# Kernel optimization log

Hardware: AMD Instinct MI355X
Metric: run time of the kernel (lower is better)

The kernel has to match this reference:

```python
import jax, jax.numpy as jnp
import numpy as np

N = 1_500_000
NUM_VOXELS = 262_144  # static segment count (replaces torch.unique's dynamic voxel count)
VSIZE = np.array([0.32, 0.32, 0.32], np.float32)
PC_MIN = np.array([-74.88, -74.88, -2.0], np.float32)
GRID = np.array([468, 468, 32], np.int64)
BN_EPS = 1e-3


def setup_inputs() -> dict:
    rng = np.random.default_rng(0)
    # points uniformly inside the point-cloud range -> the range mask is all-true
    xyz = rng.uniform(PC_MIN, PC_MIN + VSIZE * GRID - 1e-3, size=(N, 3)).astype(np.float32)
    feats = rng.uniform(0.0, 1.0, size=(N, 1)).astype(np.float32)
    coords = np.floor((xyz - PC_MIN) / VSIZE).astype(np.int64)
    merge = coords[:, 0] * (GRID[1] * GRID[2]) + coords[:, 1] * GRID[2] + coords[:, 2]
    unq_inv = (merge % NUM_VOXELS).astype(np.int32)  # static-size stand-in for unique inverse ids
    key = jax.random.key(0)
    k1, k2 = jax.random.split(key)
    return {
        'points_xyz': jnp.asarray(xyz),
        'point_feats': jnp.asarray(feats),
        'w1': jax.random.normal(k1, (11, 32), jnp.float32) * 0.1,
        'g1': jnp.ones((32,), jnp.float32),
        'b1': jnp.zeros((32,), jnp.float32),
        'w2': jax.random.normal(k2, (64, 64), jnp.float32) * 0.1,
        'g2': jnp.ones((64,), jnp.float32),
        'b2': jnp.zeros((64,), jnp.float32),
        'unq_inv': jnp.asarray(unq_inv),
    }


def _pfn(x, w, g, b, unq_inv):
    # Linear(bias=False) -> BatchNorm1d(train-mode batch stats, eps=1e-3) -> ReLU -> scatter_max
    y = x @ w
    mu = jnp.mean(y, axis=0)
    var = jnp.var(y, axis=0)
    y = (y - mu) * jax.lax.rsqrt(var + BN_EPS) * g + b
    y = jax.nn.relu(y)
    # relu output >= 0; clamp empty segments (-inf) to 0, matching torch_scatter's zero fill
    y_max = jnp.maximum(jax.ops.segment_max(y, unq_inv, num_segments=NUM_VOXELS), 0.0)
    return y, y_max


def reference(points_xyz, point_feats, w1, g1, b1, w2, g2, b2, unq_inv):
    vsize = jnp.asarray(VSIZE)
    pc_min = jnp.asarray(PC_MIN)
    coords = jnp.floor((points_xyz - pc_min) / vsize)  # [N,3] float voxel coords

    # scatter_mean of xyz per voxel -> cluster-relative offsets
    ones = jnp.ones((points_xyz.shape[0],), points_xyz.dtype)
    cnt = jax.ops.segment_sum(ones, unq_inv, num_segments=NUM_VOXELS)
    vsum = jax.ops.segment_sum(points_xyz, unq_inv, num_segments=NUM_VOXELS)
    vmean = vsum / jnp.maximum(cnt, 1.0)[:, None]
    f_cluster = points_xyz - vmean[unq_inv]

    # offset from voxel center
    f_center = points_xyz - (coords * vsize + vsize * 0.5 + pc_min)
    dist = jnp.linalg.norm(points_xyz, axis=1, keepdims=True)

    feat = jnp.concatenate([points_xyz, point_feats, f_cluster, f_center, dist], axis=-1)  # [N,11]

    x, x_max = _pfn(feat, w1, g1, b1, unq_inv)            # [N,32], [V,32]
    x = jnp.concatenate([x, x_max[unq_inv]], axis=1)       # [N,64]
    _, out = _pfn(x, w2, g2, b2, unq_inv)                  # [V,64] pillar features
    return out
```

## Files before the change

### kernel.cpp

```cpp
#include <hip/hip_runtime.h>

#define NPTS 1500000
#define NVOX 262144
#define BN_EPS 1e-3f
#define PAD 1500160
#define NB_PT 5860
#define NB_L2 11720

typedef __attribute__((ext_vector_type(8))) short bf16x8;
typedef __attribute__((ext_vector_type(4))) float f32x4;

__device__ __forceinline__ unsigned fkey(float f) {
    unsigned u = __float_as_uint(f);
    return u ^ ((unsigned)(((int)u) >> 31) | 0x80000000u);
}
__device__ __forceinline__ float funkey(unsigned k) {
    unsigned u = (k & 0x80000000u) ? (k ^ 0x80000000u) : ~k;
    return __uint_as_float(u);
}
#define KEY_NEG_INF 0x007FFFFFu

__device__ __forceinline__ float bf2f(unsigned short h) {
    union { unsigned u; float f; } x; x.u = ((unsigned)h) << 16; return x.f;
}
__device__ __forceinline__ unsigned short f2bf(float f) {
    union { float f; unsigned u; } x; x.f = f;
    unsigned r = x.u + 0x7FFFu + ((x.u >> 16) & 1u);
    return (unsigned short)(r >> 16);
}

__device__ __forceinline__ void make_feat(float x, float y, float z, float w,
                                          float mx, float my, float mz, float* f) {
    const float VS = 0.32f;
    const float PMX = -74.88f, PMY = -74.88f, PMZ = -2.0f;
    f[0] = x; f[1] = y; f[2] = z; f[3] = w;
    f[4] = x - mx; f[5] = y - my; f[6] = z - mz;
    float cx = floorf((x - PMX) / VS);
    float cy = floorf((y - PMY) / VS);
    float cz = floorf((z - PMZ) / VS);
    f[7] = x - (cx * VS + 0.5f * VS + PMX);
    f[8] = y - (cy * VS + 0.5f * VS + PMY);
    f[9] = z - (cz * VS + 0.5f * VS + PMZ);
    f[10] = sqrtf(x * x + y * y + z * z);
}

__global__ void k_init(unsigned* __restrict__ okeys, unsigned* __restrict__ xmraw,
                       int* __restrict__ cntv, float* __restrict__ zf,
                       int* __restrict__ svid, const float* __restrict__ w2,
                       uint4* __restrict__ wfrag) {
    long t0 = (long)blockIdx.x * 256 + threadIdx.x;
    long st = (long)gridDim.x * 256;
    uint4 kneg = make_uint4(KEY_NEG_INF, KEY_NEG_INF, KEY_NEG_INF, KEY_NEG_INF);
    for (long i = t0; i < (long)NVOX * 16; i += st) ((uint4*)okeys)[i] = kneg;
    for (long i = t0; i < (long)NVOX * 8; i += st) ((uint4*)xmraw)[i] = kneg;
    for (long i = t0; i < NVOX / 4; i += st) ((int4*)cntv)[i] = make_int4(0, 0, 0, 0);
    for (long i = t0; i < (1024 + 256 * 64 + 256 * 128) / 4; i += st)
        ((float4*)zf)[i] = make_float4(0.f, 0.f, 0.f, 0.f);
    if (t0 < PAD - NPTS) svid[NPTS + t0] = -1;
    if (blockIdx.x == 0 && threadIdx.x < 64) {
        int l = threadIdx.x;
        int lr = l & 15, lk = l >> 4;
        #pragma unroll
        for (int nt = 0; nt < 4; ++nt)
            #pragma unroll
            for (int kt = 0; kt < 2; ++kt) {
                int col = nt * 16 + lr;
                int kb = kt * 32 + lk * 8;
                unsigned u[4];
                #pragma unroll
                for (int j = 0; j < 4; ++j) {
                    float a = w2[(kb + 2 * j) * 64 + col];
                    float b = w2[(kb + 2 * j + 1) * 64 + col];
                    u[j] = (unsigned)f2bf(a) | ((unsigned)f2bf(b) << 16);
                }
                wfrag[(nt * 2 + kt) * 64 + l] = make_uint4(u[0], u[1], u[2], u[3]);
            }
    }
}

__global__ void k_hist(const int* __restrict__ unq, int* __restrict__ cntv) {
    int i = blockIdx.x * blockDim.x + threadIdx.x;
    if (i < NPTS) atomicAdd(&cntv[unq[i]], 1);
}

__global__ void k_scanA(const int* __restrict__ cntv, int* __restrict__ startv,
                        int* __restrict__ bsum) {
    __shared__ int lds[256];
    int t = threadIdx.x;
    int idx4 = blockIdx.x * 256 + t;
    int4 cv = ((const int4*)cntv)[idx4];
    int s0 = cv.x, s1 = s0 + cv.y, s2 = s1 + cv.z, T = s2 + cv.w;
    lds[t] = T;
    __syncthreads();
    for (int o = 1; o < 256; o <<= 1) {
        int v = (t >= o) ? lds[t - o] : 0;
        __syncthreads();
        lds[t] += v;
        __syncthreads();
    }
    int excl = lds[t] - T;
    int4 ov; ov.x = excl; ov.y = excl + s0; ov.z = excl + s1; ov.w = excl + s2;
    ((int4*)startv)[idx4] = ov;
    if (t == 255) bsum[blockIdx.x] = lds[255];
}

__global__ void k_scanB(int* __restrict__ bsum) {
    __shared__ int lds[256];
    int t = threadIdx.x;
    int b = bsum[t];
    lds[t] = b;
    __syncthreads();
    for (int o = 1; o < 256; o <<= 1) {
        int v = (t >= o) ? lds[t - o] : 0;
        __syncthreads();
        lds[t] += v;
        __syncthreads();
    }
    bsum[t] = lds[t] - b;
}

__global__ void k_scanC(int* __restrict__ startv, int* __restrict__ offv,
                        const int* __restrict__ bsum) {
    int t = threadIdx.x;
    int idx4 = blockIdx.x * 256 + t;
    int add = bsum[blockIdx.x];
    int4 v = ((int4*)startv)[idx4];
    v.x += add; v.y += add; v.z += add; v.w += add;
    ((int4*)startv)[idx4] = v;
    ((int4*)offv)[idx4] = v;
}

__global__ void k_scatter2(const float* __restrict__ xyz, const float* __restrict__ pf,
                           const int* __restrict__ unq, int* __restrict__ offv,
                           float4* __restrict__ spts, int* __restrict__ svid) {
    int i = blockIdx.x * blockDim.x + threadIdx.x;
    if (i >= NPTS) return;
    int v = unq[i];
    int pos = atomicAdd(&offv[v], 1);
    float4 p;
    p.x = xyz[3 * i + 0]; p.y = xyz[3 * i + 1]; p.z = xyz[3 * i + 2]; p.w = pf[i];
    spts[pos] = p;
    svid[pos] = v;
}

__global__ void k_vmean2(const float4* __restrict__ spts, const int* __restrict__ cntv,
                         const int* __restrict__ startv, float4* __restrict__ vmeanv) {
    int v = blockIdx.x * 256 + threadIdx.x;
    int cnt = cntv[v];
    if (!cnt) return;
    int st = startv[v];
    float sx = 0, sy = 0, sz = 0;
    for (int j = 0; j < cnt; ++j) {
        float4 p = spts[st + j];
        sx += p.x; sy += p.y; sz += p.z;
    }
    float inv = 1.0f / (float)cnt;
    vmeanv[v] = make_float4(sx * inv, sy * inv, sz * inv, 0.f);
}

__device__ __forceinline__ void flush32(int v, float m, bool atom, int c,
                                        unsigned* __restrict__ xm) {
    if ((unsigned)v >= (unsigned)NVOX) return;
    if (atom) atomicMax(&xm[(size_t)v * 32 + c], fkey(m));
    else xm[(size_t)v * 32 + c] = fkey(m);
}
__device__ __forceinline__ void flush64(int v, float m, bool atom, int c,
                                        unsigned* __restrict__ ok) {
    if ((unsigned)v >= (unsigned)NVOX) return;
    if (atom) atomicMax(&ok[(size_t)v * 64 + c], fkey(m));
    else ok[(size_t)v * 64 + c] = fkey(m);
}

__global__ __launch_bounds__(256) void k_passA(
    const float4* __restrict__ spts, const int* __restrict__ svid,
    const float4* __restrict__ vmeanv, const float* __restrict__ w1,
    unsigned* __restrict__ xmraw, float* __restrict__ spart1) {
    __shared__ float ylds[256 * 32];
    __shared__ int vlds[256];
    __shared__ float accs[64];
    __shared__ int hv[8][32]; __shared__ float hk[8][32];
    __shared__ int tv[8][32]; __shared__ float tk[8][32];
    __shared__ unsigned char sgl[8][32];
    int t = threadIdx.x;
    if (t < 64) accs[t] = 0.f;
    long grow = (long)blockIdx.x * 256 + t;
    int vid = (grow < NPTS) ? svid[grow] : -1;
    vlds[t] = vid;
    float yv[32];
    #pragma unroll
    for (int c = 0; c < 32; ++c) yv[c] = 0.f;
    if (vid >= 0) {
        float4 p = spts[grow];
        float4 vm = vmeanv[vid];
        float f[11];
        make_feat(p.x, p.y, p.z, p.w, vm.x, vm.y, vm.z, f);
        #pragma unroll
        for (int k = 0; k < 11; ++k) {
            float fk = f[k];
            #pragma unroll
            for (int c = 0; c < 32; ++c) yv[c] = fmaf(fk, w1[k * 32 + c], yv[c]);
        }
    }
    f32x4* yr = (f32x4*)&ylds[t * 32];
    #pragma unroll
    for (int q = 0; q < 8; ++q) {
        f32x4 vv = {yv[4 * q], yv[4 * q + 1], yv[4 * q + 2], yv[4 * q + 3]};
        yr[q ^ (t & 7)] = vv;
    }
    __syncthreads();
    {
        int c = t & 31, ck = t >> 5;
        int cq = c >> 2, ce = c & 3;
        float sa = 0.f, sq = 0.f;
        int cur_v = -2; float cur_m = 0.f;
        int hvv = -2; float hkk = 0.f; bool fd = false;
        for (int s = 0; s < 32; ++s) {
            int r = ck * 32 + s;
            float y = ylds[r * 32 + 4 * (cq ^ (r & 7)) + ce];
            int v = vlds[r];
            sa += y; sq += y * y;
            if (s == 0) { cur_v = v; cur_m = y; }
            else if (v == cur_v) cur_m = fmaxf(cur_m, y);
            else {
                if (!fd) { hvv = cur_v; hkk = cur_m; fd = true; }
                else if ((unsigned)cur_v < (unsigned)NVOX)
                    xmraw[(size_t)cur_v * 32 + c] = fkey(cur_m);
                cur_v = v; cur_m = y;
            }
        }
        hv[ck][c] = fd ? hvv : cur_v; hk[ck][c] = fd ? hkk : cur_m;
        tv[ck][c] = cur_v; tk[ck][c] = cur_m; sgl[ck][c] = fd ? 0 : 1;
        atomicAdd(&accs[c], sa);
        atomicAdd(&accs[32 + c], sq);
    }
    __syncthreads();
    if (t < 32) {
        int cv = hv[0][t]; float cm = hk[0][t]; bool fs = true;
        #pragma unroll
        for (int k2 = 0; k2 < 8; ++k2) {
            if (k2 > 0) {
                int nv = hv[k2][t]; float nm = hk[k2][t];
                if (nv == cv) cm = fmaxf(cm, nm);
                else { flush32(cv, cm, fs, t, xmraw); cv = nv; cm = nm; fs = false; }
            }
            if (!sgl[k2][t]) {
                flush32(cv, cm, fs, t, xmraw);
                cv = tv[k2][t]; cm = tk[k2][t]; fs = false;
            }
        }
        flush32(cv, cm, true, t, xmraw);
    }
    if (t < 64) atomicAdd(&spart1[(blockIdx.x & 255) * 64 + t], accs[t]);
}

__global__ void k_fin1(const float* __restrict__ spart1, float* __restrict__ stats,
                       const float* __restrict__ g1, const float* __restrict__ b1) {
    __shared__ float cs[64];
    int t = threadIdx.x;
    float s = 0.f;
    for (int r = 0; r < 256; ++r) s += spart1[r * 64 + t];
    cs[t] = s;
    __syncthreads();
    if (t < 32) {
        float invn = 1.0f / (float)NPTS;
        float mu = cs[t] * invn;
        float var = cs[32 + t] * invn - mu * mu;
        float sc = rsqrtf(var + BN_EPS) * g1[t];
        stats[64 + t] = sc;
        stats[96 + t] = b1[t] - mu * sc;
    }
}

__global__ __launch_bounds__(256) void k_l2(
    const float4* __restrict__ spts, const int* __restrict__ svid,
    const float4* __restrict__ vmeanv, const float* __restrict__ w1,
    const unsigned* __restrict__ xmraw, const uint4* __restrict__ wfrag,
    const float* __restrict__ stats, float* __restrict__ spart2,
    unsigned* __restrict__ okeys) {
    __shared__ unsigned y2t[64 * 64];
    __shared__ float wsums[4][128];
    __shared__ int hv[4][64]; __shared__ float hk[4][64];
    __shared__ int tv[4][64]; __shared__ float tk[4][64];
    __shared__ unsigned char sgl[4][64];

    int t = threadIdx.x;
    int lane = t & 63, wave = t >> 6;
    int lr = lane & 15, lk = lane >> 4;
    int wbase = wave * 32;
    long brow = (long)blockIdx.x * 128;

    float sc1[8], sh1[8];
    {
        float4 a0 = ((const float4*)(stats + 64))[lk * 2];
        float4 a1 = ((const float4*)(stats + 64))[lk * 2 + 1];
        float4 b0 = ((const float4*)(stats + 96))[lk * 2];
        float4 b1_ = ((const float4*)(stats + 96))[lk * 2 + 1];
        sc1[0] = a0.x; sc1[1] = a0.y; sc1[2] = a0.z; sc1[3] = a0.w;
        sc1[4] = a1.x; sc1[5] = a1.y; sc1[6] = a1.z; sc1[7] = a1.w;
        sh1[0] = b0.x; sh1[1] = b0.y; sh1[2] = b0.z; sh1[3] = b0.w;
        sh1[4] = b1_.x; sh1[5] = b1_.y; sh1[6] = b1_.z; sh1[7] = b1_.w;
    }
    int vid_l = svid[brow + wbase + (lane & 31)];

    uint4 bw[8];
    #pragma unroll
    for (int q = 0; q < 8; ++q) bw[q] = wfrag[q * 64 + lane];

    bf16x8 afr[2][2];
    #pragma unroll
    for (int mt = 0; mt < 2; ++mt) {
        int riw = mt * 16 + lr;
        int vid = __shfl(vid_l, riw);
        long grow = brow + wbase + riw;
        unsigned packz[4], packx[4];
        if (vid >= 0) {
            float4 p = spts[grow];
            float4 vm = vmeanv[vid];
            float f[11];
            make_feat(p.x, p.y, p.z, p.w, vm.x, vm.y, vm.z, f);
            float yv[8];
            #pragma unroll
            for (int j = 0; j < 8; ++j) yv[j] = 0.f;
            const float4* w1f = (const float4*)w1;
            #pragma unroll
            for (int k = 0; k < 11; ++k) {
                float4 wa = w1f[k * 8 + lk * 2];
                float4 wb = w1f[k * 8 + lk * 2 + 1];
                float fk = f[k];
                yv[0] = fmaf(fk, wa.x, yv[0]); yv[1] = fmaf(fk, wa.y, yv[1]);
                yv[2] = fmaf(fk, wa.z, yv[2]); yv[3] = fmaf(fk, wa.w, yv[3]);
                yv[4] = fmaf(fk, wb.x, yv[4]); yv[5] = fmaf(fk, wb.y, yv[5]);
                yv[6] = fmaf(fk, wb.z, yv[6]); yv[7] = fmaf(fk, wb.w, yv[7]);
            }
            const uint4* xr = (const uint4*)(xmraw + (size_t)vid * 32);
            uint4 x0 = xr[lk * 2], x1 = xr[lk * 2 + 1];
            float xs[8] = {funkey(x0.x), funkey(x0.y), funkey(x0.z), funkey(x0.w),
                           funkey(x1.x), funkey(x1.y), funkey(x1.z), funkey(x1.w)};
            #pragma unroll
            for (int e = 0; e < 4; ++e) {
                float z0 = fmaxf(0.f, fmaf(yv[2 * e], sc1[2 * e], sh1[2 * e]));
                float z1 = fmaxf(0.f, fmaf(yv[2 * e + 1], sc1[2 * e + 1], sh1[2 * e + 1]));
                packz[e] = (unsigned)f2bf(z0) | ((unsigned)f2bf(z1) << 16);
                float q0 = fmaxf(0.f, fmaf(xs[2 * e], sc1[2 * e], sh1[2 * e]));
                float q1 = fmaxf(0.f, fmaf(xs[2 * e + 1], sc1[2 * e + 1], sh1[2 * e + 1]));
                packx[e] = (unsigned)f2bf(q0) | ((unsigned)f2bf(q1) << 16);
            }
        } else {
            #pragma unroll
            for (int e = 0; e < 4; ++e) { packz[e] = 0u; packx[e] = 0u; }
        }
        afr[mt][0] = __builtin_bit_cast(bf16x8, make_uint4(packz[0], packz[1], packz[2], packz[3]));
        afr[mt][1] = __builtin_bit_cast(bf16x8, make_uint4(packx[0], packx[1], packx[2], packx[3]));
    }

    f32x4 acc[2][4];
    #pragma unroll
    for (int mt = 0; mt < 2; ++mt)
        #pragma unroll
        for (int nt = 0; nt < 4; ++nt) {
            acc[mt][nt] = (f32x4){0.f, 0.f, 0.f, 0.f};
            #pragma unroll
            for (int kt = 0; kt < 2; ++kt)
                acc[mt][nt] = __builtin_amdgcn_mfma_f32_16x16x32_bf16(
                    afr[mt][kt], __builtin_bit_cast(bf16x8, bw[nt * 2 + kt]),
                    acc[mt][nt], 0, 0, 0);
        }

    {
        float sa[4] = {0.f, 0.f, 0.f, 0.f}, sq[4] = {0.f, 0.f, 0.f, 0.f};
        #pragma unroll
        for (int mt = 0; mt < 2; ++mt)
            #pragma unroll
            for (int nt = 0; nt < 4; ++nt)
                #pragma unroll
                for (int e = 0; e < 4; ++e) {
                    float v = acc[mt][nt][e];
                    sa[nt] += v; sq[nt] += v * v;
                }
        #pragma unroll
        for (int nt = 0; nt < 4; ++nt) {
            sa[nt] += __shfl_xor(sa[nt], 16); sa[nt] += __shfl_xor(sa[nt], 32);
            sq[nt] += __shfl_xor(sq[nt], 16); sq[nt] += __shfl_xor(sq[nt], 32);
        }
        if (lk == 0) {
            #pragma unroll
            for (int nt = 0; nt < 4; ++nt) {
                wsums[wave][nt * 16 + lr] = sa[nt];
                wsums[wave][64 + nt * 16 + lr] = sq[nt];
            }
        }
    }

    #pragma unroll
    for (int mt = 0; mt < 2; ++mt)
        #pragma unroll
        for (int nt = 0; nt < 4; ++nt) {
            int col = nt * 16 + lr;
            int w0 = (wbase + mt * 16 + lk * 4) >> 1;
            unsigned u0 = (unsigned)f2bf(acc[mt][nt][0]) | ((unsigned)f2bf(acc[mt][nt][1]) << 16);
            unsigned u1 = (unsigned)f2bf(acc[mt][nt][2]) | ((unsigned)f2bf(acc[mt][nt][3]) << 16);
            y2t[col * 64 + (w0 ^ (col & 31))] = u0;
            y2t[col * 64 + ((w0 + 1) ^ (col & 31))] = u1;
        }

    {
        int c = lane;
        int cur_v = -2; float cur_m = 0.f;
        int hvv = -2; float hkk = 0.f; bool fd = false;
        for (int q = 0; q < 16; ++q) {
            unsigned u = y2t[c * 64 + (((wbase >> 1) + q) ^ (c & 31))];
            #pragma unroll
            for (int e = 0; e < 2; ++e) {
                float d = bf2f((unsigned short)(e ? (u >> 16) : (u & 0xFFFF)));
                int v = __shfl(vid_l, 2 * q + e);
                if (q == 0 && e == 0) { cur_v = v; cur_m = d; }
                else if (v == cur_v) cur_m = fmaxf(cur_m, d);
                else {
                    if (!fd) { hvv = cur_v; hkk = cur_m; fd = true; }
                    else if ((unsigned)cur_v < (unsigned)NVOX)
                        okeys[(size_t)cur_v * 64 + c] = fkey(cur_m);
                    cur_v = v; cur_m = d;
                }
            }
        }
        hv[wave][c] = fd ? hvv : cur_v; hk[wave][c] = fd ? hkk : cur_m;
        tv[wave][c] = cur_v; tk[wave][c] = cur_m; sgl[wave][c] = fd ? 0 : 1;
    }
    __syncthreads();
    if (t < 64) {
        int cv = hv[0][t]; float cm = hk[0][t]; bool fs = true;
        #pragma unroll
        for (int k2 = 0; k2 < 4; ++k2) {
            if (k2 > 0) {
                int nv = hv[k2][t]; float nm = hk[k2][t];
                if (nv == cv) cm = fmaxf(cm, nm);
                else { flush64(cv, cm, fs, t, okeys); cv = nv; cm = nm; fs = false; }
            }
            if (!sgl[k2][t]) {
                flush64(cv, cm, fs, t, okeys);
                cv = tv[k2][t]; cm = tk[k2][t]; fs = false;
            }
        }
        flush64(cv, cm, true, t, okeys);
    }
    if (t < 128) {
        float s = wsums[0][t] + wsums[1][t] + wsums[2][t] + wsums[3][t];
        atomicAdd(&spart2[(blockIdx.x & 255) * 128 + t], s);
    }
}

__global__ void k_fin2(const float* __restrict__ spart2, float* __restrict__ stats,
                       const float* __restrict__ g2, const float* __restrict__ b2) {
    __shared__ float cs[128];
    int t = threadIdx.x;
    float s = 0.f;
    for (int r = 0; r < 256; ++r) s += spart2[r * 128 + t];
    cs[t] = s;
    __syncthreads();
    if (t < 64) {
        float invn = 1.0f / (float)NPTS;
        float mu = cs[t] * invn;
        float var = cs[64 + t] * invn - mu * mu;
        float sc = rsqrtf(var + BN_EPS) * g2[t];
        stats[256 + t] = sc;
        stats[320 + t] = b2[t] - mu * sc;
    }
}

__global__ void k_out(unsigned* __restrict__ okeys, const float* __restrict__ stats) {
    int i4 = blockIdx.x * 256 + threadIdx.x;
    uint4 u = ((const uint4*)okeys)[i4];
    int c0 = (i4 & 15) * 4;
    float4 o;
    o.x = fmaxf(0.f, fmaf(funkey(u.x), stats[256 + c0 + 0], stats[320 + c0 + 0]));
    o.y = fmaxf(0.f, fmaf(funkey(u.y), stats[256 + c0 + 1], stats[320 + c0 + 1]));
    o.z = fmaxf(0.f, fmaf(funkey(u.z), stats[256 + c0 + 2], stats[320 + c0 + 2]));
    o.w = fmaxf(0.f, fmaf(funkey(u.w), stats[256 + c0 + 3], stats[320 + c0 + 3]));
    ((float4*)okeys)[i4] = o;
}

extern "C" void kernel_launch(void* const* d_in, const int* in_sizes, int n_in,
                              void* d_out, int out_size, void* d_ws, size_t ws_size,
                              hipStream_t stream) {
    const float* xyz = (const float*)d_in[0];
    const float* pf  = (const float*)d_in[1];
    const float* w1  = (const float*)d_in[2];
    const float* g1  = (const float*)d_in[3];
    const float* b1  = (const float*)d_in[4];
    const float* w2  = (const float*)d_in[5];
    const float* g2  = (const float*)d_in[6];
    const float* b2  = (const float*)d_in[7];
    const int*   unq = (const int*)d_in[8];

    float4* spts     = (float4*)d_ws;
    float4* vmeanv   = spts + PAD;
    int* svid        = (int*)(vmeanv + NVOX);
    unsigned* xmraw  = (unsigned*)(svid + PAD);
    int* cntv        = (int*)(xmraw + (size_t)NVOX * 32);
    int* startv      = cntv + NVOX;
    int* offv        = startv + NVOX;
    int* bsum        = offv + NVOX;
    float* stats     = (float*)(bsum + 256);
    float* spart1    = stats + 1024;
    float* spart2    = spart1 + 256 * 64;
    uint4* wfrag     = (uint4*)(spart2 + 256 * 128);

    unsigned* okeys = (unsigned*)d_out;

    k_init<<<2048, 256, 0, stream>>>(okeys, xmraw, cntv, stats, svid, w2, wfrag);
    k_hist<<<NB_PT, 256, 0, stream>>>(unq, cntv);
    k_scanA<<<256, 256, 0, stream>>>(cntv, startv, bsum);
    k_scanB<<<1, 256, 0, stream>>>(bsum);
    k_scanC<<<256, 256, 0, stream>>>(startv, offv, bsum);
    k_scatter2<<<NB_PT, 256, 0, stream>>>(xyz, pf, unq, offv, spts, svid);
    k_vmean2<<<NVOX / 256, 256, 0, stream>>>(spts, cntv, startv, vmeanv);
    k_passA<<<NB_PT, 256, 0, stream>>>(spts, svid, vmeanv, w1, xmraw, spart1);
    k_fin1<<<1, 64, 0, stream>>>(spart1, stats, g1, b1);
    k_l2<<<NB_L2, 256, 0, stream>>>(spts, svid, vmeanv, w1, xmraw, wfrag, stats,
                                    spart2, okeys);
    k_fin2<<<1, 128, 0, stream>>>(spart2, stats, g2, b2);
    k_out<<<NVOX * 16 / 256, 256, 0, stream>>>(okeys, stats);
}
```

Before: 460.7 us.

## Make passA and layer-2 per-wave independent, removing block barriers and LDS merges

k_passA now processes 128 points per block with each wave handling 32 rows split across two half-waves, so each lane computes 16 channels instead of 32. Run-length segment-max merging moves from a block-wide LDS/__syncthreads merge to per-wave flushes that use atomics at boundaries. k_l2 computes the layer-1 features once per row (split across half-waves) and stages them through a swizzled per-wave LDS buffer to form MFMA A fragments, instead of recomputing them per fragment lane. BN partial sums go straight to global atomics per wave. This removes block barriers and redundant feature math, at the cost of more global atomic flushes.

```diff
diff --git a/kernel.cpp b/kernel.cpp
--- a/kernel.cpp
+++ b/kernel.cpp
@@ -27,6 +27,9 @@
     union { float f; unsigned u; } x; x.f = f;
     unsigned r = x.u + 0x7FFFu + ((x.u >> 16) & 1u);
     return (unsigned short)(r >> 16);
+}
+__device__ __forceinline__ unsigned packbf(float a, float b) {
+    return (unsigned)f2bf(a) | ((unsigned)f2bf(b) << 16);
 }
 
 __device__ __forceinline__ void make_feat(float x, float y, float z, float w,
@@ -71,7 +74,7 @@
                 for (int j = 0; j < 4; ++j) {
                     float a = w2[(kb + 2 * j) * 64 + col];
                     float b = w2[(kb + 2 * j + 1) * 64 + col];
-                    u[j] = (unsigned)f2bf(a) | ((unsigned)f2bf(b) << 16);
+                    u[j] = packbf(a, b);
                 }
                 wfrag[(nt * 2 + kt) * 64 + l] = make_uint4(u[0], u[1], u[2], u[3]);
             }
@@ -175,82 +178,63 @@
     const float4* __restrict__ spts, const int* __restrict__ svid,
     const float4* __restrict__ vmeanv, const float* __restrict__ w1,
     unsigned* __restrict__ xmraw, float* __restrict__ spart1) {
-    __shared__ float ylds[256 * 32];
-    __shared__ int vlds[256];
-    __shared__ float accs[64];
-    __shared__ int hv[8][32]; __shared__ float hk[8][32];
-    __shared__ int tv[8][32]; __shared__ float tk[8][32];
-    __shared__ unsigned char sgl[8][32];
-    int t = threadIdx.x;
-    if (t < 64) accs[t] = 0.f;
-    long grow = (long)blockIdx.x * 256 + t;
-    int vid = (grow < NPTS) ? svid[grow] : -1;
-    vlds[t] = vid;
-    float yv[32];
-    #pragma unroll
-    for (int c = 0; c < 32; ++c) yv[c] = 0.f;
+    __shared__ float ylds[4][32 * 33];
+    int t = threadIdx.x;
+    int lane = t & 63, wave = t >> 6;
+    int rl = lane & 31, half = lane >> 5;
+    long grow = (long)blockIdx.x * 128 + wave * 32 + rl;
+    int vid = svid[grow];
+    float yv[16];
+    #pragma unroll
+    for (int j = 0; j < 16; ++j) yv[j] = 0.f;
     if (vid >= 0) {
         float4 p = spts[grow];
         float4 vm = vmeanv[vid];
         float f[11];
         make_feat(p.x, p.y, p.z, p.w, vm.x, vm.y, vm.z, f);
+        const float4* w1f = (const float4*)w1;
         #pragma unroll
         for (int k = 0; k < 11; ++k) {
             float fk = f[k];
             #pragma unroll
-            for (int c = 0; c < 32; ++c) yv[c] = fmaf(fk, w1[k * 32 + c], yv[c]);
-        }
-    }
-    f32x4* yr = (f32x4*)&ylds[t * 32];
-    #pragma unroll
-    for (int q = 0; q < 8; ++q) {
-        f32x4 vv = {yv[4 * q], yv[4 * q + 1], yv[4 * q + 2], yv[4 * q + 3]};
-        yr[q ^ (t & 7)] = vv;
-    }
-    __syncthreads();
-    {
-        int c = t & 31, ck = t >> 5;
-        int cq = c >> 2, ce = c & 3;
-        float sa = 0.f, sq = 0.f;
-        int cur_v = -2; float cur_m = 0.f;
-        int hvv = -2; float hkk = 0.f; bool fd = false;
-        for (int s = 0; s < 32; ++s) {
-            int r = ck * 32 + s;
-            float y = ylds[r * 32 + 4 * (cq ^ (r & 7)) + ce];
-            int v = vlds[r];
-            sa += y; sq += y * y;
-            if (s == 0) { cur_v = v; cur_m = y; }
-            else if (v == cur_v) cur_m = fmaxf(cur_m, y);
-            else {
-                if (!fd) { hvv = cur_v; hkk = cur_m; fd = true; }
-                else if ((unsigned)cur_v < (unsigned)NVOX)
-                    xmraw[(size_t)cur_v * 32 + c] = fkey(cur_m);
-                cur_v = v; cur_m = y;
+            for (int q = 0; q < 4; ++q) {
+                float4 wq = w1f[k * 8 + half * 4 + q];
+                yv[4 * q + 0] = fmaf(fk, wq.x, yv[4 * q + 0]);
+                yv[4 * q + 1] = fmaf(fk, wq.y, yv[4 * q + 1]);
+                yv[4 * q + 2] = fmaf(fk, wq.z, yv[4 * q + 2]);
+                yv[4 * q + 3] = fmaf(fk, wq.w, yv[4 * q + 3]);
             }
         }
-        hv[ck][c] = fd ? hvv : cur_v; hk[ck][c] = fd ? hkk : cur_m;
-        tv[ck][c] = cur_v; tk[ck][c] = cur_m; sgl[ck][c] = fd ? 0 : 1;
-        atomicAdd(&accs[c], sa);
-        atomicAdd(&accs[32 + c], sq);
-    }
-    __syncthreads();
-    if (t < 32) {
-        int cv = hv[0][t]; float cm = hk[0][t]; bool fs = true;
-        #pragma unroll
-        for (int k2 = 0; k2 < 8; ++k2) {
-            if (k2 > 0) {
-                int nv = hv[k2][t]; float nm = hk[k2][t];
-                if (nv == cv) cm = fmaxf(cm, nm);
-                else { flush32(cv, cm, fs, t, xmraw); cv = nv; cm = nm; fs = false; }
-            }
-            if (!sgl[k2][t]) {
-                flush32(cv, cm, fs, t, xmraw);
-                cv = tv[k2][t]; cm = tk[k2][t]; fs = false;
-            }
-        }
-        flush32(cv, cm, true, t, xmraw);
-    }
-    if (t < 64) atomicAdd(&spart1[(blockIdx.x & 255) * 64 + t], accs[t]);
+    }
+    float* yw = &ylds[wave][0];
+    #pragma unroll
+    for (int j = 0; j < 16; ++j) yw[rl * 33 + half * 16 + j] = yv[j];
+    asm volatile("s_waitcnt lgkmcnt(0)" ::: "memory");
+    __builtin_amdgcn_sched_barrier(0);
+    int c = rl;
+    float sa = 0.f, sq = 0.f;
+    int cur_v = -2; float cur_m = 0.f; bool first = true;
+    #pragma unroll
+    for (int i = 0; i < 16; ++i) {
+        int r = half * 16 + i;
+        float y = yw[r * 33 + c];
+        int v = __shfl(vid, r);
+        sa += y; sq += y * y;
+        if (i == 0) { cur_v = v; cur_m = y; }
+        else if (v == cur_v) cur_m = fmaxf(cur_m, y);
+        else {
+            flush32(cur_v, cur_m, first, c, xmraw);
+            first = false; cur_v = v; cur_m = y;
+        }
+    }
+    flush32(cur_v, cur_m, true, c, xmraw);
+    sa += __shfl_xor(sa, 32);
+    sq += __shfl_xor(sq, 32);
+    if (half == 0) {
+        int slot = (blockIdx.x * 4 + wave) & 255;
+        atomicAdd(&spart1[slot * 64 + c], sa);
+        atomicAdd(&spart1[slot * 64 + 32 + c], sq);
+    }
 }
 
 __global__ void k_fin1(const float* __restrict__ spart1, float* __restrict__ stats,
@@ -277,30 +261,73 @@
     const unsigned* __restrict__ xmraw, const uint4* __restrict__ wfrag,
     const float* __restrict__ stats, float* __restrict__ spart2,
     unsigned* __restrict__ okeys) {
-    __shared__ unsigned y2t[64 * 64];
-    __shared__ float wsums[4][128];
-    __shared__ int hv[4][64]; __shared__ float hk[4][64];
-    __shared__ int tv[4][64]; __shared__ float tk[4][64];
-    __shared__ unsigned char sgl[4][64];
-
+    __shared__ unsigned Abuf[4][32 * 32];
+    __shared__ unsigned y2t[4][64 * 17];
     int t = threadIdx.x;
     int lane = t & 63, wave = t >> 6;
+    int rl = lane & 31, half = lane >> 5;
     int lr = lane & 15, lk = lane >> 4;
-    int wbase = wave * 32;
-    long brow = (long)blockIdx.x * 128;
-
-    float sc1[8], sh1[8];
+    long brow = (long)blockIdx.x * 128 + wave * 32;
+    int vid = svid[brow + rl];
+
+    unsigned zpk[8], xpk[8];
+    if (vid >= 0) {
+        float4 p = spts[brow + rl];
+        float4 vm = vmeanv[vid];
+        float f[11];
+        make_feat(p.x, p.y, p.z, p.w, vm.x, vm.y, vm.z, f);
+        float yv[16];
+        #pragma unroll
+        for (int j = 0; j < 16; ++j) yv[j] = 0.f;
+        const float4* w1f = (const float4*)w1;
+        #pragma unroll
+        for (int k = 0; k < 11; ++k) {
+            float fk = f[k];
+            #pragma unroll
+            for (int q = 0; q < 4; ++q) {
+                float4 wq = w1f[k * 8 + half * 4 + q];
+                yv[4 * q + 0] = fmaf(fk, wq.x, yv[4 * q + 0]);
+                yv[4 * q + 1] = fmaf(fk, wq.y, yv[4 * q + 1]);
+                yv[4 * q + 2] = fmaf(fk, wq.z, yv[4 * q + 2]);
+                yv[4 * q + 3] = fmaf(fk, wq.w, yv[4 * q + 3]);
+            }
+        }
+        const uint4* xr = (const uint4*)(xmraw + (size_t)vid * 32);
+        uint4 xq[4];
+        #pragma unroll
+        for (int q = 0; q < 4; ++q) xq[q] = xr[half * 4 + q];
+        const unsigned* xu = (const unsigned*)xq;
+        #pragma unroll
+        for (int q = 0; q < 4; ++q) {
+            float4 sc = ((const float4*)(stats + 64))[half * 4 + q];
+            float4 sh = ((const float4*)(stats + 96))[half * 4 + q];
+            float z0 = fmaxf(0.f, fmaf(yv[4 * q + 0], sc.x, sh.x));
+            float z1 = fmaxf(0.f, fmaf(yv[4 * q + 1], sc.y, sh.y));
+            float z2 = fmaxf(0.f, fmaf(yv[4 * q + 2], sc.z, sh.z));
+            float z3 = fmaxf(0.f, fmaf(yv[4 * q + 3], sc.w, sh.w));
+            zpk[2 * q + 0] = packbf(z0, z1);
+            zpk[2 * q + 1] = packbf(z2, z3);
+            float x0 = fmaxf(0.f, fmaf(funkey(xu[4 * q + 0]), sc.x, sh.x));
+            float x1 = fmaxf(0.f, fmaf(funkey(xu[4 * q + 1]), sc.y, sh.y));
+            float x2 = fmaxf(0.f, fmaf(funkey(xu[4 * q + 2]), sc.z, sh.z));
+            float x3 = fmaxf(0.f, fmaf(funkey(xu[4 * q + 3]), sc.w, sh.w));
+            xpk[2 * q + 0] = packbf(x0, x1);
+            xpk[2 * q + 1] = packbf(x2, x3);
+        }
+    } else {
+        #pragma unroll
+        for (int q = 0; q < 8; ++q) { zpk[q] = 0u; xpk[q] = 0u; }
+    }
     {
-        float4 a0 = ((const float4*)(stats + 64))[lk * 2];
-        float4 a1 = ((const float4*)(stats + 64))[lk * 2 + 1];
-        float4 b0 = ((const float4*)(stats + 96))[lk * 2];
-        float4 b1_ = ((const float4*)(stats + 96))[lk * 2 + 1];
-        sc1[0] = a0.x; sc1[1] = a0.y; sc1[2] = a0.z; sc1[3] = a0.w;
-        sc1[4] = a1.x; sc1[5] = a1.y; sc1[6] = a1.z; sc1[7] = a1.w;
-        sh1[0] = b0.x; sh1[1] = b0.y; sh1[2] = b0.z; sh1[3] = b0.w;
-        sh1[4] = b1_.x; sh1[5] = b1_.y; sh1[6] = b1_.z; sh1[7] = b1_.w;
-    }
-    int vid_l = svid[brow + wbase + (lane & 31)];
+        uint4* arow = (uint4*)&Abuf[wave][rl * 32];
+        int sw = rl & 7;
+        arow[(2 * half + 0) ^ sw] = *(const uint4*)&zpk[0];
+        arow[(2 * half + 1) ^ sw] = *(const uint4*)&zpk[4];
+        arow[(4 + 2 * half) ^ sw] = *(const uint4*)&xpk[0];
+        arow[(5 + 2 * half) ^ sw] = *(const uint4*)&xpk[4];
+    }
+    asm volatile("s_waitcnt lgkmcnt(0)" ::: "memory");
+    __builtin_amdgcn_sched_barrier(0);
 
     uint4 bw[8];
     #pragma unroll
@@ -308,51 +335,13 @@
 
     bf16x8 afr[2][2];
     #pragma unroll
-    for (int mt = 0; mt < 2; ++mt) {
-        int riw = mt * 16 + lr;
-        int vid = __shfl(vid_l, riw);
-        long grow = brow + wbase + riw;
-        unsigned packz[4], packx[4];
-        if (vid >= 0) {
-            float4 p = spts[grow];
-            float4 vm = vmeanv[vid];
-            float f[11];
-            make_feat(p.x, p.y, p.z, p.w, vm.x, vm.y, vm.z, f);
-            float yv[8];
-            #pragma unroll
-            for (int j = 0; j < 8; ++j) yv[j] = 0.f;
-            const float4* w1f = (const float4*)w1;
-            #pragma unroll
-            for (int k = 0; k < 11; ++k) {
-                float4 wa = w1f[k * 8 + lk * 2];
-                float4 wb = w1f[k * 8 + lk * 2 + 1];
-                float fk = f[k];
-                yv[0] = fmaf(fk, wa.x, yv[0]); yv[1] = fmaf(fk, wa.y, yv[1]);
-                yv[2] = fmaf(fk, wa.z, yv[2]); yv[3] = fmaf(fk, wa.w, yv[3]);
-                yv[4] = fmaf(fk, wb.x, yv[4]); yv[5] = fmaf(fk, wb.y, yv[5]);
-                yv[6] = fmaf(fk, wb.z, yv[6]); yv[7] = fmaf(fk, wb.w, yv[7]);
-            }
-            const uint4* xr = (const uint4*)(xmraw + (size_t)vid * 32);
-            uint4 x0 = xr[lk * 2], x1 = xr[lk * 2 + 1];
-            float xs[8] = {funkey(x0.x), funkey(x0.y), funkey(x0.z), funkey(x0.w),
-                           funkey(x1.x), funkey(x1.y), funkey(x1.z), funkey(x1.w)};
-            #pragma unroll
-            for (int e = 0; e < 4; ++e) {
-                float z0 = fmaxf(0.f, fmaf(yv[2 * e], sc1[2 * e], sh1[2 * e]));
-                float z1 = fmaxf(0.f, fmaf(yv[2 * e + 1], sc1[2 * e + 1], sh1[2 * e + 1]));
-                packz[e] = (unsigned)f2bf(z0) | ((unsigned)f2bf(z1) << 16);
-                float q0 = fmaxf(0.f, fmaf(xs[2 * e], sc1[2 * e], sh1[2 * e]));
-                float q1 = fmaxf(0.f, fmaf(xs[2 * e + 1], sc1[2 * e + 1], sh1[2 * e + 1]));
-                packx[e] = (unsigned)f2bf(q0) | ((unsigned)f2bf(q1) << 16);
-            }
-        } else {
-            #pragma unroll
-            for (int e = 0; e < 4; ++e) { packz[e] = 0u; packx[e] = 0u; }
-        }
-        afr[mt][0] = __builtin_bit_cast(bf16x8, make_uint4(packz[0], packz[1], packz[2], packz[3]));
-        afr[mt][1] = __builtin_bit_cast(bf16x8, make_uint4(packx[0], packx[1], packx[2], packx[3]));
-    }
-
+    for (int mt = 0; mt < 2; ++mt)
+        #pragma unroll
+        for (int kt = 0; kt < 2; ++kt) {
+            int riw = mt * 16 + lr;
+            uint4 uu = ((const uint4*)&Abuf[wave][riw * 32])[(kt * 4 + lk) ^ (riw & 7)];
+            afr[mt][kt] = __builtin_bit_cast(bf16x8, uu);
+        }
     f32x4 acc[2][4];
     #pragma unroll
     for (int mt = 0; mt < 2; ++mt)
@@ -364,6 +353,16 @@
                 acc[mt][nt] = __builtin_amdgcn_mfma_f32_16x16x32_bf16(
                     afr[mt][kt], __builtin_bit_cast(bf16x8, bw[nt * 2 + kt]),
                     acc[mt][nt], 0, 0, 0);
+        }
+
+    #pragma unroll
+    for (int mt = 0; mt < 2; ++mt)
+        #pragma unroll
+        for (int nt = 0; nt < 4; ++nt) {
+            int col = nt * 16 + lr;
+            int w0 = mt * 8 + lk * 2;
+            y2t[wave][col * 17 + w0] = packbf(acc[mt][nt][0], acc[mt][nt][1]);
+            y2t[wave][col * 17 + w0 + 1] = packbf(acc[mt][nt][2], acc[mt][nt][3]);
         }
 
     {
@@ -383,69 +382,36 @@
             sq[nt] += __shfl_xor(sq[nt], 16); sq[nt] += __shfl_xor(sq[nt], 32);
         }
         if (lk == 0) {
+            int slot = (blockIdx.x * 4 + wave) & 255;
             #pragma unroll
             for (int nt = 0; nt < 4; ++nt) {
-                wsums[wave][nt * 16 + lr] = sa[nt];
-                wsums[wave][64 + nt * 16 + lr] = sq[nt];
+                atomicAdd(&spart2[slot * 128 + nt * 16 + lr], sa[nt]);
+                atomicAdd(&spart2[slot * 128 + 64 + nt * 16 + lr], sq[nt]);
             }
         }
     }
-
-    #pragma unroll
-    for (int mt = 0; mt < 2; ++mt)
-        #pragma unroll
-        for (int nt = 0; nt < 4; ++nt) {
-            int col = nt * 16 + lr;
-            int w0 = (wbase + mt * 16 + lk * 4) >> 1;
-            unsigned u0 = (unsigned)f2bf(acc[mt][nt][0]) | ((unsigned)f2bf(acc[mt][nt][1]) << 16);
-            unsigned u1 = (unsigned)f2bf(acc[mt][nt][2]) | ((unsigned)f2bf(acc[mt][nt][3]) << 16);
-            y2t[col * 64 + (w0 ^ (col & 31))] = u0;
-            y2t[col * 64 + ((w0 + 1) ^ (col & 31))] = u1;
-        }
+    asm volatile("s_waitcnt lgkmcnt(0)" ::: "memory");
+    __builtin_amdgcn_sched_barrier(0);
 
     {
         int c = lane;
-        int cur_v = -2; float cur_m = 0.f;
-        int hvv = -2; float hkk = 0.f; bool fd = false;
+        int cur_v = -2; float cur_m = 0.f; bool first = true;
+        #pragma unroll
         for (int q = 0; q < 16; ++q) {
-            unsigned u = y2t[c * 64 + (((wbase >> 1) + q) ^ (c & 31))];
+            unsigned u = y2t[wave][c * 17 + q];
             #pragma unroll
             for (int e = 0; e < 2; ++e) {
                 float d = bf2f((unsigned short)(e ? (u >> 16) : (u & 0xFFFF)));
-                int v = __shfl(vid_l, 2 * q + e);
+                int v = __shfl(vid, 2 * q + e);
                 if (q == 0 && e == 0) { cur_v = v; cur_m = d; }
                 else if (v == cur_v) cur_m = fmaxf(cur_m, d);
                 else {
-                    if (!fd) { hvv = cur_v; hkk = cur_m; fd = true; }
-                    else if ((unsigned)cur_v < (unsigned)NVOX)
-                        okeys[(size_t)cur_v * 64 + c] = fkey(cur_m);
-                    cur_v = v; cur_m = d;
+                    flush64(cur_v, cur_m, first, c, okeys);
+                    first = false; cur_v = v; cur_m = d;
                 }
             }
         }
-        hv[wave][c] = fd ? hvv : cur_v; hk[wave][c] = fd ? hkk : cur_m;
-        tv[wave][c] = cur_v; tk[wave][c] = cur_m; sgl[wave][c] = fd ? 0 : 1;
-    }
-    __syncthreads();
-    if (t < 64) {
-        int cv = hv[0][t]; float cm = hk[0][t]; bool fs = true;
-        #pragma unroll
-        for (int k2 = 0; k2 < 4; ++k2) {
-            if (k2 > 0) {
-                int nv = hv[k2][t]; float nm = hk[k2][t];
-                if (nv == cv) cm = fmaxf(cm, nm);
-                else { flush64(cv, cm, fs, t, okeys); cv = nv; cm = nm; fs = false; }
-            }
-            if (!sgl[k2][t]) {
-                flush64(cv, cm, fs, t, okeys);
-                cv = tv[k2][t]; cm = tk[k2][t]; fs = false;
-            }
-        }
-        flush64(cv, cm, true, t, okeys);
-    }
-    if (t < 128) {
-        float s = wsums[0][t] + wsums[1][t] + wsums[2][t] + wsums[3][t];
-        atomicAdd(&spart2[(blockIdx.x & 255) * 128 + t], s);
+        flush64(cur_v, cur_m, true, c, okeys);
     }
 }
 
@@ -514,7 +480,7 @@
     k_scanC<<<256, 256, 0, stream>>>(startv, offv, bsum);
     k_scatter2<<<NB_PT, 256, 0, stream>>>(xyz, pf, unq, offv, spts, svid);
     k_vmean2<<<NVOX / 256, 256, 0, stream>>>(spts, cntv, startv, vmeanv);
-    k_passA<<<NB_PT, 256, 0, stream>>>(spts, svid, vmeanv, w1, xmraw, spart1);
+    k_passA<<<NB_L2, 256, 0, stream>>>(spts, svid, vmeanv, w1, xmraw, spart1);
     k_fin1<<<1, 64, 0, stream>>>(spart1, stats, g1, b1);
     k_l2<<<NB_L2, 256, 0, stream>>>(spts, svid, vmeanv, w1, xmraw, wfrag, stats,
                                     spart2, okeys);
```

New measurement: 430.4 us. -6.6%, faster.
